# Optimization experiments

Measured on AMD Instinct MI355X. Metric: run time of the kernel, lower is better.

Reference implementation:

```python
import jax, jax.numpy as jnp
import numpy as np

TOP_K = 2          # routed top_k = top_k - num_shared_experts = 3 - 1
CAP_FACTOR = 1.1   # capacity_factor


def setup_inputs() -> dict:
    key = jax.random.key(0)
    ks = jax.random.split(key, 12)
    B, S, D, E = 4, 2048, 1024, 7
    s = 0.02
    return {
        "x": jax.random.normal(ks[0], (B, S, D), jnp.float32),
        "noise": jax.random.normal(ks[1], (B, S, E), jnp.float32),
        "Wr": jax.random.normal(ks[2], (D, E)) * s, "br": jnp.zeros((E,)),
        "Wn": jax.random.normal(ks[3], (D, E)) * s, "bn": jnp.zeros((E,)),
        "W1": jax.random.normal(ks[4], (E, D, D)) * s, "b1": jnp.zeros((E, D)),
        "W2": jax.random.normal(ks[5], (E, D, D)) * s, "b2": jnp.zeros((E, D)),
        "Ws1": jax.random.normal(ks[6], (D, D)) * s, "bs1": jnp.zeros((D,)),
        "Ws2": jax.random.normal(ks[7], (D, D)) * s, "bs2": jnp.zeros((D,)),
    }


def reference(x, noise, Wr, br, Wn, bn, W1, b1, W2, b2, Ws1, bs1, Ws2, bs2):
    B, S, D = x.shape
    E = Wr.shape[1]
    N = B * S
    C = int(N * TOP_K / E * CAP_FACTOR)  # per-expert capacity (static)

    # shared expert (Dropout inactive at inference)
    x_shared = jax.nn.relu(x @ Ws1 + bs1) @ Ws2 + bs2

    # --- noisy top-k router ---
    logits = x @ Wr + br
    noisy = logits + noise * jax.nn.softplus(x @ Wn + bn)
    vals, idx = jax.lax.top_k(noisy, TOP_K)                    # [B,S,K]
    onehot = jax.nn.one_hot(idx, E, dtype=x.dtype)             # [B,S,K,E]
    probs_k = jax.nn.softmax(vals, axis=-1)                    # softmax over -inf-masked logits == softmax over top-k vals
    router_probs = jnp.einsum('bske,bsk->bse', onehot, probs_k)
    expert_mask = onehot.sum(-2)
    lbl = E * (router_probs.mean((0, 1)) * expert_mask.mean((0, 1))).sum()

    # --- capacity-limited dispatch, first-come-first-served in flat token order ---
    flat_x = x.reshape(N, D)
    flat_g = router_probs.reshape(N, E)
    m = (expert_mask.reshape(N, E) > 0).T                      # [E,N] token->expert assignment
    pos = jnp.cumsum(m.astype(jnp.int32), axis=1) - 1          # slot within expert
    valid = m & (pos < C)
    token = jnp.arange(N, dtype=jnp.int32)
    dest = jnp.where(valid, jnp.arange(E, dtype=jnp.int32)[:, None] * C + pos, E * C)
    idxs = jnp.full((E * C + 1,), N, dtype=jnp.int32)
    idxs = idxs.at[dest.reshape(-1)].set(jnp.broadcast_to(token, (E, N)).reshape(-1))
    idxs = idxs[:E * C].reshape(E, C)                          # token id per slot, N = padding

    xpad = jnp.concatenate([flat_x, jnp.zeros((1, D), x.dtype)], axis=0)
    gpad = jnp.concatenate([flat_g, jnp.zeros((1, E), x.dtype)], axis=0)
    xe = xpad[idxs]                                            # [E,C,D]
    h = jax.nn.relu(jnp.einsum('ecd,edh->ech', xe, W1) + b1[:, None, :])
    out = jnp.einsum('ech,ehd->ecd', h, W2) + b2[:, None, :]
    g = (gpad[idxs] * jnp.eye(E, dtype=x.dtype)[:, None, :]).sum(-1)  # [E,C] gate per slot
    slot_valid = (idxs < N).astype(x.dtype)
    weighted = out * (g * slot_valid)[..., None]

    upd = jnp.zeros((N + 1, D), x.dtype).at[idxs.reshape(-1)].add(weighted.reshape(-1, D))[:N]
    final = upd.reshape(B, S, D) + x_shared
    return final, lbl
```

## Files before the change

kernel.cpp:

```cpp
#include <hip/hip_runtime.h>
#include <math.h>

typedef unsigned short u16;
typedef __attribute__((ext_vector_type(4))) float f32x4;
typedef __bf16 bf16x8 __attribute__((ext_vector_type(8)));

#define NTOK 8192
#define DDIM 1024
#define NEXP 7
#define CAPC 2574
#define CPAD 2688
#define EBLK 1176
#define TBLK 1688

__device__ inline float bf2f(u16 u) {
    union { unsigned int i; float f; } c; c.i = ((unsigned int)u) << 16; return c.f;
}
__device__ inline u16 f2bf(float f) {
    union { float f; unsigned int i; } c; c.f = f;
    unsigned int u = c.i;
    unsigned int r = (u + 0x7fffu + ((u >> 16) & 1u)) >> 16;
    return (u16)r;
}

__device__ inline void gl2lds16(const u16* g, const u16* l) {
    __builtin_amdgcn_global_load_lds(
        (const __attribute__((address_space(1))) unsigned int*)g,
        (__attribute__((address_space(3))) unsigned int*)l, 16, 0, 0);
}

__global__ void k_zero(float* out, long n) {
    long i = (long)blockIdx.x * 256 + threadIdx.x;
    long stride = (long)gridDim.x * 256;
    for (; i < n; i += stride) out[i] = 0.f;
}

__global__ void k_prep(const float* __restrict__ x, u16* __restrict__ xb,
                       int* __restrict__ slot_token, u16* __restrict__ zrow,
                       const float* __restrict__ W1, const float* __restrict__ Ws1,
                       u16* __restrict__ Wt, u16* __restrict__ Wst,
                       const float* __restrict__ W2, const float* __restrict__ Ws2,
                       u16* __restrict__ Wt2, u16* __restrict__ Wst2) {
    int bid = blockIdx.x, tid = threadIdx.x;
    if (bid < 4096) {
        int gid = bid * 256 + tid;
        int i = gid * 8;
        float4 a = *(const float4*)(x + i);
        float4 b = *(const float4*)(x + i + 4);
        ushort4 o0; o0.x = f2bf(a.x); o0.y = f2bf(a.y); o0.z = f2bf(a.z); o0.w = f2bf(a.w);
        ushort4 o1; o1.x = f2bf(b.x); o1.y = f2bf(b.y); o1.z = f2bf(b.z); o1.w = f2bf(b.w);
        *(ushort4*)(xb + i) = o0;
        *(ushort4*)(xb + i + 4) = o1;
        if (gid < DDIM) zrow[gid] = 0;
        if (gid < NEXP * CPAD) slot_token[gid] = NTOK;
        return;
    }
    int phase2 = (bid >= 8192);
    int tb = bid - (phase2 ? 8192 : 4096);
    const float* srcE = phase2 ? W2 : W1;
    const float* srcS = phase2 ? Ws2 : Ws1;
    u16* dE = phase2 ? Wt2 : Wt;
    u16* dS = phase2 ? Wst2 : Wst;
    int z = tb >> 9; int rem = tb & 511;
    int y = rem >> 2; int xq = rem & 3;
    const float* src; u16* dst;
    if (z < 7) { src = srcE + (long)z * 1048576; dst = dE + (long)z * 1048576; }
    else       { src = srcS;                     dst = dS; }
    int n = xq * 256 + tid;
    int k0 = y * 8;
    u16 v[8];
#pragma unroll
    for (int j = 0; j < 8; ++j) v[j] = f2bf(src[(long)(k0 + j) * 1024 + n]);
    ushort4 a; a.x = v[0]; a.y = v[1]; a.z = v[2]; a.w = v[3];
    ushort4 b; b.x = v[4]; b.y = v[5]; b.z = v[6]; b.w = v[7];
    *(ushort4*)(dst + (long)n * 1024 + k0) = a;
    *(ushort4*)(dst + (long)n * 1024 + k0 + 4) = b;
}

__global__ void k_transpose(const float* __restrict__ srcE, const float* __restrict__ srcS,
                            u16* __restrict__ Wt, u16* __restrict__ Wst) {
    int z = blockIdx.z;
    const float* src; u16* dst;
    if (z < 7) { src = srcE + (long)z * 1048576; dst = Wt + (long)z * 1048576; }
    else       { src = srcS;                     dst = Wst; }
    int n = blockIdx.x * 256 + threadIdx.x;
    int k0 = blockIdx.y * 8;
    u16 v[8];
#pragma unroll
    for (int j = 0; j < 8; ++j) v[j] = f2bf(src[(long)(k0 + j) * 1024 + n]);
    ushort4 a; a.x = v[0]; a.y = v[1]; a.z = v[2]; a.w = v[3];
    ushort4 b; b.x = v[4]; b.y = v[5]; b.z = v[6]; b.w = v[7];
    *(ushort4*)(dst + (long)n * 1024 + k0) = a;
    *(ushort4*)(dst + (long)n * 1024 + k0 + 4) = b;
}

__global__ __launch_bounds__(512) void k_router(
    const float* __restrict__ x,
    const float* __restrict__ Wr, const float* __restrict__ Wn,
    double* __restrict__ arO, double* __restrict__ anO) {
    __shared__ float swr[7168];
    __shared__ float swn[7168];
    int tid = threadIdx.x;
    for (int i = tid; i < 7168; i += 512) { swr[i] = Wr[i]; swn[i] = Wn[i]; }
    __syncthreads();
    int lane = tid & 63, wv = tid >> 6;
    int t = blockIdx.x * 8 + wv;
    double ar[7] = {0,0,0,0,0,0,0}, an[7] = {0,0,0,0,0,0,0};
    for (int j = 0; j < 16; ++j) {
        int d = j * 64 + lane;
        double xd = (double)x[t * 1024 + d];
#pragma unroll
        for (int e = 0; e < 7; ++e) {
            ar[e] += xd * (double)swr[d * 7 + e];
            an[e] += xd * (double)swn[d * 7 + e];
        }
    }
#pragma unroll
    for (int e = 0; e < 7; ++e) {
        for (int o = 32; o > 0; o >>= 1) {
            ar[e] += __shfl_xor(ar[e], o);
            an[e] += __shfl_xor(an[e], o);
        }
    }
    if (lane == 0) {
#pragma unroll
        for (int e = 0; e < 7; ++e) { arO[t * 7 + e] = ar[e]; anO[t * 7 + e] = an[e]; }
    }
}

__global__ void k_tail(const double* __restrict__ arO, const double* __restrict__ anO,
                       const float* __restrict__ noise,
                       const float* __restrict__ br, const float* __restrict__ bn,
                       int* __restrict__ idx0, int* __restrict__ idx1,
                       float* __restrict__ p0, float* __restrict__ p1,
                       int* __restrict__ cntA, double* __restrict__ sumA) {
    int t = blockIdx.x * 256 + threadIdx.x;
    int lane = threadIdx.x & 63;
    double best = -1e300, second = -1e300; int b0 = 0, b1 = 0;
#pragma unroll
    for (int e = 0; e < 7; ++e) {
        double lg = arO[t * 7 + e] + (double)br[e];
        double z  = anO[t * 7 + e] + (double)bn[e];
        double sp = (z > 30.0) ? (z + log1p(exp(-z))) : log1p(exp(z));
        double v  = lg + (double)noise[t * 7 + e] * sp;
        if (v > best)        { second = best; b1 = b0; best = v; b0 = e; }
        else if (v > second) { second = v; b1 = e; }
    }
    double ex = exp(second - best);
    float q0 = (float)(1.0 / (1.0 + ex));
    float q1 = (float)(ex / (1.0 + ex));
    idx0[t] = b0; idx1[t] = b1; p0[t] = q0; p1[t] = q1;
    int chunk = t >> 6;
    double dq0 = (double)q0, dq1 = (double)q1;
#pragma unroll
    for (int e = 0; e < 7; ++e) {
        unsigned long long m = __ballot((b0 == e) || (b1 == e));
        double q = (b0 == e ? dq0 : 0.0) + (b1 == e ? dq1 : 0.0);
        for (int o = 32; o > 0; o >>= 1) q += __shfl_xor(q, o);
        if (lane == 0) { cntA[e * 128 + chunk] = __popcll(m); sumA[e * 128 + chunk] = q; }
    }
}

__global__ void k_scanbase(const int* __restrict__ cntA, const double* __restrict__ sumA,
                           int* __restrict__ baseA, int* __restrict__ cnt,
                           float* __restrict__ out) {
    __shared__ int s[128];
    __shared__ double rd[128];
    __shared__ int rawc[7];
    __shared__ double ps[7];
    int tid = threadIdx.x;
    for (int e = 0; e < 7; ++e) {
        int v = 0;
        if (tid < 128) { v = cntA[e * 128 + tid]; s[tid] = v; }
        if (tid < 128) rd[tid] = sumA[e * 128 + tid];
        __syncthreads();
        for (int o = 1; o < 128; o <<= 1) {
            int add = 0;
            if (tid < 128 && tid >= o) add = s[tid - o];
            __syncthreads();
            if (tid < 128) s[tid] += add;
            __syncthreads();
        }
        if (tid < 128) baseA[e * 128 + tid] = s[tid] - v;
        if (tid == 127) { rawc[e] = s[127]; cnt[e] = (s[127] < CAPC) ? s[127] : CAPC; }
        for (int o = 64; o > 0; o >>= 1) {
            if (tid < o) rd[tid] += rd[tid + o];
            __syncthreads();
        }
        if (tid == 0) ps[e] = rd[0];
        __syncthreads();
    }
    if (tid == 0) {
        double acc = 0.0;
        for (int e = 0; e < 7; ++e) acc += ps[e] * (double)rawc[e];
        out[(long)NTOK * DDIM] = (float)(7.0 * acc / (8192.0 * 8192.0));
    }
}

__global__ void k_assign(const int* __restrict__ idx0, const int* __restrict__ idx1,
                         const int* __restrict__ baseA, int* __restrict__ slot_token,
                         int* __restrict__ ts0, int* __restrict__ ts1) {
    int lane = threadIdx.x & 63;
    int chunk = (blockIdx.x * 256 + threadIdx.x) >> 6;
    int t = chunk * 64 + lane;
    int i0 = idx0[t], i1 = idx1[t];
    int myts0 = -1, myts1 = -1;
    unsigned long long lt = (1ull << lane) - 1ull;
#pragma unroll
    for (int e = 0; e < 7; ++e) {
        bool has = (i0 == e) || (i1 == e);
        unsigned long long m = __ballot(has);
        int pre = __popcll(m & lt);
        int pos = baseA[e * 128 + chunk] + pre;
        if (has && pos < CAPC) {
            int slot = e * CPAD + pos;
            slot_token[slot] = t;
            if (i0 == e) myts0 = slot; else myts1 = slot;
        }
    }
    ts0[t] = myts0; ts1[t] = myts1;
}

template <bool GATHER, bool MODE_H>
__global__ __launch_bounds__(256) void k_gemm(
    const u16* __restrict__ AbaseE, const u16* __restrict__ AbaseS,
    const int* __restrict__ gidx, const u16* __restrict__ zrow,
    const u16* __restrict__ WtE, const u16* __restrict__ WtS,
    const float* __restrict__ biasE, const float* __restrict__ biasS,
    u16* __restrict__ outE, u16* __restrict__ outS,
    const int* __restrict__ cnt) {
    __shared__ __align__(16) u16 ldsA[128 * 64];
    __shared__ __align__(16) u16 ldsB[128 * 64];
    int bid = blockIdx.x;
    int tid = threadIdx.x, lane = tid & 63, wv = tid >> 6;
    int lrow = lane >> 3, lkg = lane & 7;
    int kgs = lkg ^ lrow;

    int e = 0, my, nx;
    const u16* Ab; const u16* Bb; const float* bias; u16* outp;
    bool gather = false;
    if (bid < EBLK) {
        e = bid / 168; int r = bid % 168; my = r >> 3; nx = r & 7;
        if (my * 128 >= cnt[e]) return;
        Ab = AbaseE + (GATHER ? 0L : (long)e * CPAD * 1024);
        Bb = WtE + ((long)e << 20);
        bias = biasE + e * 1024;
        outp = outE + (long)e * CPAD * 1024;
        gather = GATHER;
    } else {
        int sb = bid - EBLK; my = sb >> 3; nx = sb & 7;
        Ab = AbaseS; Bb = WtS; bias = biasS; outp = outS;
    }
    int m0 = my * 128, n0 = nx * 128;

    const u16* arow[4];
    const u16* brow[4];
#pragma unroll
    for (int i = 0; i < 4; ++i) {
        int r = (wv * 4 + i) * 8 + lrow;
        if (gather) {
            int tok = gidx[e * CPAD + m0 + r];
            arow[i] = (tok < NTOK) ? (AbaseE + (long)tok * DDIM) : zrow;
        } else {
            arow[i] = Ab + (long)(m0 + r) * DDIM;
        }
        brow[i] = Bb + (long)(n0 + r) * DDIM;
    }
    f32x4 acc[4][4];
#pragma unroll
    for (int a = 0; a < 4; ++a)
#pragma unroll
        for (int b = 0; b < 4; ++b) { f32x4 z = {0.f, 0.f, 0.f, 0.f}; acc[a][b] = z; }

    int wm = (wv >> 1) * 64, wn = (wv & 1) * 64;
    int rl = lane & 15, quad = lane >> 4;

    for (int k0 = 0; k0 < 1024; k0 += 64) {
#pragma unroll
        for (int i = 0; i < 4; ++i) {
            gl2lds16(arow[i] + k0 + kgs * 8, &ldsA[(wv * 4 + i) * 512]);
            gl2lds16(brow[i] + k0 + kgs * 8, &ldsB[(wv * 4 + i) * 512]);
        }
        __syncthreads();
#pragma unroll
        for (int ks = 0; ks < 2; ++ks) {
            int kg = ks * 4 + quad;
            bf16x8 af[4], bf[4];
#pragma unroll
            for (int mi = 0; mi < 4; ++mi) {
                int row = wm + mi * 16 + rl;
                af[mi] = *(const bf16x8*)&ldsA[row * 64 + (kg ^ (row & 7)) * 8];
            }
#pragma unroll
            for (int ni = 0; ni < 4; ++ni) {
                int row = wn + ni * 16 + rl;
                bf[ni] = *(const bf16x8*)&ldsB[row * 64 + (kg ^ (row & 7)) * 8];
            }
#pragma unroll
            for (int mi = 0; mi < 4; ++mi)
#pragma unroll
                for (int ni = 0; ni < 4; ++ni)
                    acc[mi][ni] = __builtin_amdgcn_mfma_f32_16x16x32_bf16(
                        af[mi], bf[ni], acc[mi][ni], 0, 0, 0);
        }
        __syncthreads();
    }
#pragma unroll
    for (int ni = 0; ni < 4; ++ni) {
        int col = n0 + wn + ni * 16 + rl;
        float bv = bias[col];
#pragma unroll
        for (int mi = 0; mi < 4; ++mi) {
            int rowb = m0 + wm + mi * 16 + quad * 4;
#pragma unroll
            for (int r = 0; r < 4; ++r) {
                float v = acc[mi][ni][r] + bv;
                if constexpr (MODE_H) v = v > 0.f ? v : 0.f;
                outp[(long)(rowb + r) * DDIM + col] = f2bf(v);
            }
        }
    }
}

__global__ __launch_bounds__(256) void k_combine(
    const u16* __restrict__ Xs, const u16* __restrict__ OutE,
    const int* __restrict__ ts0, const int* __restrict__ ts1,
    const float* __restrict__ p0, const float* __restrict__ p1,
    float* __restrict__ out) {
    int b = blockIdx.x;
    int d = threadIdx.x * 4;
    long base = (long)b * DDIM + d;
    ushort4 xs4 = *(const ushort4*)(Xs + base);
    float r0 = bf2f(xs4.x), r1 = bf2f(xs4.y), r2 = bf2f(xs4.z), r3 = bf2f(xs4.w);
    int s0 = ts0[b], s1 = ts1[b];
    if (s0 >= 0) {
        float g = p0[b];
        ushort4 o4 = *(const ushort4*)(OutE + (long)s0 * DDIM + d);
        r0 += g * bf2f(o4.x); r1 += g * bf2f(o4.y); r2 += g * bf2f(o4.z); r3 += g * bf2f(o4.w);
    }
    if (s1 >= 0) {
        float g = p1[b];
        ushort4 o4 = *(const ushort4*)(OutE + (long)s1 * DDIM + d);
        r0 += g * bf2f(o4.x); r1 += g * bf2f(o4.y); r2 += g * bf2f(o4.z); r3 += g * bf2f(o4.w);
    }
    float4 w; w.x = r0; w.y = r1; w.z = r2; w.w = r3;
    *(float4*)(out + base) = w;
}

extern "C" void kernel_launch(void* const* d_in, const int* in_sizes, int n_in,
                              void* d_out, int out_size, void* d_ws, size_t ws_size,
                              hipStream_t stream) {
    const float* x    = (const float*)d_in[0];
    const float* noise= (const float*)d_in[1];
    const float* Wr   = (const float*)d_in[2];
    const float* br   = (const float*)d_in[3];
    const float* Wn   = (const float*)d_in[4];
    const float* bn   = (const float*)d_in[5];
    const float* W1   = (const float*)d_in[6];
    const float* b1   = (const float*)d_in[7];
    const float* W2   = (const float*)d_in[8];
    const float* b2   = (const float*)d_in[9];
    const float* Ws1  = (const float*)d_in[10];
    const float* bs1  = (const float*)d_in[11];
    const float* Ws2  = (const float*)d_in[12];
    const float* bs2  = (const float*)d_in[13];
    float* out = (float*)d_out;
    char* ws = (char*)d_ws;

    size_t off = 0;
    auto alloc = [&](size_t bytes) { size_t o = off; off += (bytes + 255) & ~(size_t)255; return o; };
    u16*  Wt   = (u16*)(ws + alloc(7ull * 1048576 * 2));
    u16*  Wst  = (u16*)(ws + alloc(1048576ull * 2));
    u16*  xb   = (u16*)(ws + alloc((size_t)NTOK * 1024 * 2));
    u16*  He   = (u16*)(ws + alloc((size_t)NEXP * CPAD * 1024 * 2));
    u16*  Hs   = (u16*)(ws + alloc((size_t)NTOK * 1024 * 2));
    u16*  OutE = (u16*)(ws + alloc((size_t)NEXP * CPAD * 1024 * 2));
    u16*  Xs   = (u16*)(ws + alloc((size_t)NTOK * 1024 * 2));
    int*  idx0 = (int*)(ws + alloc(NTOK * 4));
    int*  idx1 = (int*)(ws + alloc(NTOK * 4));
    float* p0  = (float*)(ws + alloc(NTOK * 4));
    float* p1  = (float*)(ws + alloc(NTOK * 4));
    int*  ts0  = (int*)(ws + alloc(NTOK * 4));
    int*  ts1  = (int*)(ws + alloc(NTOK * 4));
    int*  slot_token = (int*)(ws + alloc(NEXP * CPAD * 4));
    int*  cntA = (int*)(ws + alloc(7 * 128 * 4));
    int*  baseA= (int*)(ws + alloc(7 * 128 * 4));
    double* sumA = (double*)(ws + alloc(7 * 128 * 8));
    int*  cnt    = (int*)(ws + alloc(8 * 4));
    u16*  zrow   = (u16*)(ws + alloc(1024 * 2));
    double* arO  = (double*)(ws + alloc((size_t)NTOK * 7 * 8));
    double* anO  = (double*)(ws + alloc((size_t)NTOK * 7 * 8));
    size_t base_off = off;
    u16*  Wt2  = (u16*)(ws + alloc(7ull * 1048576 * 2));
    u16*  Wst2 = (u16*)(ws + alloc(1048576ull * 2));

    if (base_off > ws_size) {
        k_zero<<<2048, 256, 0, stream>>>(out, (long)out_size);
        return;
    }
    bool sep = (off <= ws_size);
    if (!sep) { Wt2 = Wt; Wst2 = Wst; }

    k_prep<<<sep ? 12288 : 8192, 256, 0, stream>>>(
        x, xb, slot_token, zrow, W1, Ws1, Wt, Wst, W2, Ws2, Wt2, Wst2);
    k_router<<<1024, 512, 0, stream>>>(x, Wr, Wn, arO, anO);
    k_tail<<<32, 256, 0, stream>>>(arO, anO, noise, br, bn, idx0, idx1, p0, p1, cntA, sumA);
    k_scanbase<<<1, 256, 0, stream>>>(cntA, sumA, baseA, cnt, out);
    k_assign<<<32, 256, 0, stream>>>(idx0, idx1, baseA, slot_token, ts0, ts1);

    k_gemm<true, true><<<TBLK, 256, 0, stream>>>(
        xb, xb, slot_token, zrow, Wt, Wst, b1, bs1, He, Hs, cnt);

    if (!sep)
        k_transpose<<<dim3(4, 128, 8), 256, 0, stream>>>(W2, Ws2, Wt, Wst);

    k_gemm<false, false><<<TBLK, 256, 0, stream>>>(
        He, Hs, nullptr, zrow, Wt2, Wst2, b2, bs2, OutE, Xs, cnt);

    k_combine<<<NTOK, 256, 0, stream>>>(Xs, OutE, ts0, ts1, p0, p1, out);
    (void)in_sizes; (void)n_in; (void)out_size;
}
```

Measured before the change: 401.1 us.

## Replace grouped GEMM with 256x256-tile, 8-wave, double-buffered LDS pipeline

The expert and shared-expert GEMM now uses 256x256 output tiles, 512 threads and a 128KB double-buffered dynamic LDS region. Global-to-LDS loads for the next K step are issued between quadrant-wise MFMA phases, and s_setprio boosts priority during the MFMA bursts. The larger tiles raise arithmetic intensity and cut the number of blocks, while the pipelining aims to hide load latency behind compute. In exchange, padding waste on partial expert tiles grows, rows must be bounds-checked, and occupancy is reduced by the large LDS use.

```diff
diff --git a/kernel.cpp b/kernel.cpp
--- a/kernel.cpp
+++ b/kernel.cpp
@@ -10,8 +10,9 @@
 #define NEXP 7
 #define CAPC 2574
 #define CPAD 2688
-#define EBLK 1176
-#define TBLK 1688
+#define MBE8 11
+#define EB8 (NEXP * MBE8 * 4)
+#define TB8 (EB8 + 32 * 4)
 
 __device__ inline float bf2f(u16 u) {
     union { unsigned int i; float f; } c; c.i = ((unsigned int)u) << 16; return c.f;
@@ -28,6 +29,9 @@
         (const __attribute__((address_space(1))) unsigned int*)g,
         (__attribute__((address_space(3))) unsigned int*)l, 16, 0, 0);
 }
+
+#define BAR()    asm volatile("s_barrier" ::: "memory")
+#define WAITV0() asm volatile("s_waitcnt vmcnt(0)" ::: "memory")
 
 __global__ void k_zero(float* out, long n) {
     long i = (long)blockIdx.x * 256 + threadIdx.x;
@@ -52,7 +56,7 @@
         *(ushort4*)(xb + i) = o0;
         *(ushort4*)(xb + i + 4) = o1;
         if (gid < DDIM) zrow[gid] = 0;
-        if (gid < NEXP * CPAD) slot_token[gid] = NTOK;
+        if (gid < NEXP * CPAD + 128) slot_token[gid] = NTOK;
         return;
     }
     int phase2 = (bid >= 8192);
@@ -221,37 +225,67 @@
     ts0[t] = myts0; ts1[t] = myts1;
 }
 
+
+#define READ_A(MQ)                                                                      \
+    _Pragma("unroll")                                                                   \
+    for (int j = 0; j < 4; ++j) {                                                       \
+        int row_ = wm * 128 + (MQ) * 64 + j * 16 + rl;                                  \
+        _Pragma("unroll")                                                               \
+        for (int kh = 0; kh < 2; ++kh)                                                  \
+            af[j][kh] = *(const bf16x8*)&sA[row_ * 64 + (((kh * 4 + quad) ^ kq7)) * 8]; \
+    }
+
+#define READ_B(NQ)                                                                      \
+    _Pragma("unroll")                                                                   \
+    for (int j = 0; j < 2; ++j) {                                                       \
+        int row_ = wn * 64 + (NQ) * 32 + j * 16 + rl;                                   \
+        _Pragma("unroll")                                                               \
+        for (int kh = 0; kh < 2; ++kh)                                                  \
+            bf[j][kh] = *(const bf16x8*)&sB[row_ * 64 + (((kh * 4 + quad) ^ kq7)) * 8]; \
+    }
+
+#define MFMA_Q(MQ, NQ)                                                                  \
+    _Pragma("unroll")                                                                   \
+    for (int kh = 0; kh < 2; ++kh)                                                      \
+        _Pragma("unroll")                                                               \
+        for (int j = 0; j < 4; ++j)                                                     \
+            _Pragma("unroll")                                                           \
+            for (int i = 0; i < 2; ++i)                                                 \
+                acc[(MQ) * 4 + j][(NQ) * 2 + i] =                                       \
+                    __builtin_amdgcn_mfma_f32_16x16x32_bf16(                            \
+                        af[j][kh], bf[i][kh], acc[(MQ) * 4 + j][(NQ) * 2 + i], 0, 0, 0);
+
 template <bool GATHER, bool MODE_H>
-__global__ __launch_bounds__(256) void k_gemm(
+__global__ __launch_bounds__(512, 2) void k_gemm8(
     const u16* __restrict__ AbaseE, const u16* __restrict__ AbaseS,
     const int* __restrict__ gidx, const u16* __restrict__ zrow,
     const u16* __restrict__ WtE, const u16* __restrict__ WtS,
     const float* __restrict__ biasE, const float* __restrict__ biasS,
     u16* __restrict__ outE, u16* __restrict__ outS,
     const int* __restrict__ cnt) {
-    __shared__ __align__(16) u16 ldsA[128 * 64];
-    __shared__ __align__(16) u16 ldsB[128 * 64];
+    extern __shared__ __align__(16) u16 lds[];
     int bid = blockIdx.x;
     int tid = threadIdx.x, lane = tid & 63, wv = tid >> 6;
-    int lrow = lane >> 3, lkg = lane & 7;
-    int kgs = lkg ^ lrow;
-
-    int e = 0, my, nx;
+    int lrow = lane >> 3, lkg = lane & 7, kgs = lkg ^ lrow;
+
+    int e = 0, my, nx, mbound;
     const u16* Ab; const u16* Bb; const float* bias; u16* outp;
     bool gather = false;
-    if (bid < EBLK) {
-        e = bid / 168; int r = bid % 168; my = r >> 3; nx = r & 7;
-        if (my * 128 >= cnt[e]) return;
-        Ab = AbaseE + (GATHER ? 0L : (long)e * CPAD * 1024);
+    if (bid < EB8) {
+        e = bid / 44; int r = bid % 44; my = r >> 2; nx = r & 3;
+        if (my * 256 >= cnt[e]) return;
+        Ab = GATHER ? AbaseE : (AbaseE + (long)e * CPAD * 1024);
         Bb = WtE + ((long)e << 20);
         bias = biasE + e * 1024;
         outp = outE + (long)e * CPAD * 1024;
         gather = GATHER;
+        mbound = CPAD;
     } else {
-        int sb = bid - EBLK; my = sb >> 3; nx = sb & 7;
+        int sb = bid - EB8; my = sb >> 2; nx = sb & 3;
         Ab = AbaseS; Bb = WtS; bias = biasS; outp = outS;
-    }
-    int m0 = my * 128, n0 = nx * 128;
+        mbound = NTOK;
+    }
+    int m0 = my * 256, n0 = nx * 256;
 
     const u16* arow[4];
     const u16* brow[4];
@@ -262,61 +296,92 @@
             int tok = gidx[e * CPAD + m0 + r];
             arow[i] = (tok < NTOK) ? (AbaseE + (long)tok * DDIM) : zrow;
         } else {
-            arow[i] = Ab + (long)(m0 + r) * DDIM;
+            int rr = m0 + r; if (rr >= mbound) rr = 0;
+            arow[i] = Ab + (long)rr * DDIM;
         }
         brow[i] = Bb + (long)(n0 + r) * DDIM;
     }
-    f32x4 acc[4][4];
-#pragma unroll
-    for (int a = 0; a < 4; ++a)
+
+    f32x4 acc[8][4];
+#pragma unroll
+    for (int a = 0; a < 8; ++a)
 #pragma unroll
         for (int b = 0; b < 4; ++b) { f32x4 z = {0.f, 0.f, 0.f, 0.f}; acc[a][b] = z; }
 
-    int wm = (wv >> 1) * 64, wn = (wv & 1) * 64;
-    int rl = lane & 15, quad = lane >> 4;
-
-    for (int k0 = 0; k0 < 1024; k0 += 64) {
-#pragma unroll
-        for (int i = 0; i < 4; ++i) {
-            gl2lds16(arow[i] + k0 + kgs * 8, &ldsA[(wv * 4 + i) * 512]);
-            gl2lds16(brow[i] + k0 + kgs * 8, &ldsB[(wv * 4 + i) * 512]);
-        }
-        __syncthreads();
-#pragma unroll
-        for (int ks = 0; ks < 2; ++ks) {
-            int kg = ks * 4 + quad;
-            bf16x8 af[4], bf[4];
-#pragma unroll
-            for (int mi = 0; mi < 4; ++mi) {
-                int row = wm + mi * 16 + rl;
-                af[mi] = *(const bf16x8*)&ldsA[row * 64 + (kg ^ (row & 7)) * 8];
-            }
-#pragma unroll
-            for (int ni = 0; ni < 4; ++ni) {
-                int row = wn + ni * 16 + rl;
-                bf[ni] = *(const bf16x8*)&ldsB[row * 64 + (kg ^ (row & 7)) * 8];
-            }
-#pragma unroll
-            for (int mi = 0; mi < 4; ++mi)
-#pragma unroll
-                for (int ni = 0; ni < 4; ++ni)
-                    acc[mi][ni] = __builtin_amdgcn_mfma_f32_16x16x32_bf16(
-                        af[mi], bf[ni], acc[mi][ni], 0, 0, 0);
-        }
-        __syncthreads();
-    }
+    int rl = lane & 15, quad = lane >> 4, kq7 = rl & 7;
+    int wm = wv >> 2, wn = wv & 3;
+    u16* s0 = lds;
+    u16* s1 = lds + 32768;
+
+#pragma unroll
+    for (int i = 0; i < 4; ++i) {
+        gl2lds16(arow[i] + kgs * 8, s0 + (wv * 4 + i) * 512);
+        gl2lds16(brow[i] + kgs * 8, s0 + 16384 + (wv * 4 + i) * 512);
+    }
+    WAITV0();
+    BAR();
+
+    bf16x8 af[4][2], bf[2][2];
+    for (int T = 0; T < 16; ++T) {
+        u16* sc = (T & 1) ? s1 : s0;
+        u16* sn = (T & 1) ? s0 : s1;
+        const u16* sA = sc;
+        const u16* sB = sc + 16384;
+        int k1 = (T + 1) * 64;
+        READ_A(0)
+        READ_B(0)
+        if (T < 15) {
+#pragma unroll
+            for (int i = 0; i < 4; ++i)
+                gl2lds16(arow[i] + k1 + kgs * 8, sn + (wv * 4 + i) * 512);
+        }
+        BAR();
+        __builtin_amdgcn_s_setprio(1);
+        MFMA_Q(0, 0)
+        __builtin_amdgcn_s_setprio(0);
+        BAR();
+        READ_B(1)
+        if (T < 15) {
+#pragma unroll
+            for (int i = 0; i < 4; ++i)
+                gl2lds16(brow[i] + k1 + kgs * 8, sn + 16384 + (wv * 4 + i) * 512);
+        }
+        BAR();
+        __builtin_amdgcn_s_setprio(1);
+        MFMA_Q(0, 1)
+        __builtin_amdgcn_s_setprio(0);
+        BAR();
+        READ_A(1)
+        BAR();
+        __builtin_amdgcn_s_setprio(1);
+        MFMA_Q(1, 1)
+        __builtin_amdgcn_s_setprio(0);
+        BAR();
+        READ_B(0)
+        BAR();
+        __builtin_amdgcn_s_setprio(1);
+        MFMA_Q(1, 0)
+        __builtin_amdgcn_s_setprio(0);
+        WAITV0();
+        BAR();
+        __builtin_amdgcn_sched_barrier(0);
+    }
+
 #pragma unroll
     for (int ni = 0; ni < 4; ++ni) {
-        int col = n0 + wn + ni * 16 + rl;
+        int col = n0 + wn * 64 + ni * 16 + rl;
         float bv = bias[col];
 #pragma unroll
-        for (int mi = 0; mi < 4; ++mi) {
-            int rowb = m0 + wm + mi * 16 + quad * 4;
+        for (int mi = 0; mi < 8; ++mi) {
+            int rowb = m0 + wm * 128 + mi * 16 + quad * 4;
 #pragma unroll
             for (int r = 0; r < 4; ++r) {
-                float v = acc[mi][ni][r] + bv;
-                if constexpr (MODE_H) v = v > 0.f ? v : 0.f;
-                outp[(long)(rowb + r) * DDIM + col] = f2bf(v);
+                int rowg = rowb + r;
+                if (rowg < mbound) {
+                    float v = acc[mi][ni][r] + bv;
+                    if constexpr (MODE_H) v = v > 0.f ? v : 0.f;
+                    outp[(long)rowg * DDIM + col] = f2bf(v);
+                }
             }
         }
     }
@@ -382,7 +447,7 @@
     float* p1  = (float*)(ws + alloc(NTOK * 4));
     int*  ts0  = (int*)(ws + alloc(NTOK * 4));
     int*  ts1  = (int*)(ws + alloc(NTOK * 4));
-    int*  slot_token = (int*)(ws + alloc(NEXP * CPAD * 4));
+    int*  slot_token = (int*)(ws + alloc((NEXP * CPAD + 128) * 4));
     int*  cntA = (int*)(ws + alloc(7 * 128 * 4));
     int*  baseA= (int*)(ws + alloc(7 * 128 * 4));
     double* sumA = (double*)(ws + alloc(7 * 128 * 8));
@@ -401,6 +466,11 @@
     bool sep = (off <= ws_size);
     if (!sep) { Wt2 = Wt; Wst2 = Wst; }
 
+    (void)hipFuncSetAttribute((const void*)k_gemm8<true, true>,
+                              hipFuncAttributeMaxDynamicSharedMemorySize, 131072);
+    (void)hipFuncSetAttribute((const void*)k_gemm8<false, false>,
+                              hipFuncAttributeMaxDynamicSharedMemorySize, 131072);
+
     k_prep<<<sep ? 12288 : 8192, 256, 0, stream>>>(
         x, xb, slot_token, zrow, W1, Ws1, Wt, Wst, W2, Ws2, Wt2, Wst2);
     k_router<<<1024, 512, 0, stream>>>(x, Wr, Wn, arO, anO);
@@ -408,13 +478,13 @@
     k_scanbase<<<1, 256, 0, stream>>>(cntA, sumA, baseA, cnt, out);
     k_assign<<<32, 256, 0, stream>>>(idx0, idx1, baseA, slot_token, ts0, ts1);
 
-    k_gemm<true, true><<<TBLK, 256, 0, stream>>>(
+    k_gemm8<true, true><<<TB8, 512, 131072, stream>>>(
         xb, xb, slot_token, zrow, Wt, Wst, b1, bs1, He, Hs, cnt);
 
     if (!sep)
         k_transpose<<<dim3(4, 128, 8), 256, 0, stream>>>(W2, Ws2, Wt, Wst);
 
-    k_gemm<false, false><<<TBLK, 256, 0, stream>>>(
+    k_gemm8<false, false><<<TB8, 512, 131072, stream>>>(
         He, Hs, nullptr, zrow, Wt2, Wst2, b2, bs2, OutE, Xs, cnt);
 
     k_combine<<<NTOK, 256, 0, stream>>>(Xs, OutE, ts0, ts1, p0, p1, out);
```

Measured after the change: 435.2 us. 8.5% more time.
